# Optimization experiments

Hardware: AMD Instinct MI355X
Metric: run time of the kernel (lower is better)

The kernel has to match this reference:

```python
import jax, jax.numpy as jnp
import numpy as np

SIGMA1 = 0.1  # init kwarg s


def setup_inputs() -> dict:
    key = jax.random.key(0)
    k1, k2 = jax.random.split(key)
    N, D = 8192, 128
    fvec = jax.random.normal(k1, (N, D), dtype=jnp.float32)
    Lvec = jax.random.randint(k2, (N,), 0, 1024, dtype=jnp.int32)
    a = jnp.ones((), dtype=jnp.float32)
    return {"fvec": fvec, "Lvec": Lvec, "a": a, "IPC": 512, "bz": 8192}


def reference(fvec, Lvec, a, IPC, bz):
    # data != 'SOP' branch of HSELoss.forward (Lvec is unused on this path).
    N = fvec.shape[0]
    # F.normalize(fvec, p=2, dim=1) with eps clamp
    norm = jnp.maximum(jnp.linalg.norm(fvec, axis=1, keepdims=True), 1e-12)
    fn = fvec / norm
    # distMC: cosine-sim matmul with diagonal forced to -1
    idx = jnp.arange(N)
    Dist = (fn @ fn.T).at[idx, idx].set(-1.0)  # [N, N]

    Dd = jax.lax.stop_gradient(Dist)  # D_detach clones
    rows = idx[:, None]
    cols = idx[None, :]
    row_sel = (rows >= bz - IPC) & (rows < bz)
    # easy: mask cols [2*IPC, bz) on the last IPC rows
    easy = jnp.where(row_sel & (cols >= 2 * IPC) & (cols < bz), -1.0, Dd)
    # hard: mask cols [0, 2*IPC) and [bz-IPC, bz) on the last IPC rows
    hard_cols = (cols < 2 * IPC) | ((cols >= bz - IPC) & (cols < bz))
    hard = jnp.where(row_sel & hard_cols, -1.0, Dd)

    I_easy = jnp.argmax(easy, axis=1)  # first max index, matches torch .max(1)
    I_hard = jnp.argmax(hard, axis=1)
    VCE = Dist[idx, I_easy]
    VCH = Dist[idx, I_hard]
    T1 = jnp.stack([VCE, VCH], axis=1)[-IPC:]  # [IPC, 2]
    Prob1 = -jax.nn.log_softmax(T1 / SIGMA1, axis=1)[:, 0]
    return a * Prob1.mean()
```

## Files before the change

### kernel.cpp

```cpp
#include <hip/hip_runtime.h>
#include <hip/hip_bf16.h>
#include <math.h>

constexpr int N   = 8192;
constexpr int D   = 128;
constexpr int IPC = 512;
constexpr int BZ  = 8192;
constexpr int Q0  = BZ - IPC;
constexpr int NQ  = IPC;
constexpr int JMAX = BZ - IPC;
constexpr int JBLK = 128;
constexpr int NJB  = JMAX / JBLK;
constexpr int EASY_JB = (2 * IPC) / JBLK;
constexpr int QBLK = 64;
constexpr int NQB  = NQ / QBLK;

typedef __attribute__((ext_vector_type(8))) short short8;
typedef __attribute__((ext_vector_type(4))) float f32x4;

__global__ __launch_bounds__(256) void knorm(const float* __restrict__ f,
                                             __hip_bfloat16* __restrict__ fn) {
    int row  = (blockIdx.x * blockDim.x + threadIdx.x) >> 6;
    int lane = threadIdx.x & 63;
    const float* rp = f + (size_t)row * D;
    float2 v = *(const float2*)(rp + 2 * lane);
    float ss = v.x * v.x + v.y * v.y;
    #pragma unroll
    for (int off = 32; off > 0; off >>= 1) ss += __shfl_xor(ss, off, 64);
    float r = 1.0f / fmaxf(sqrtf(ss), 1e-12f);
    __hip_bfloat162 h;
    h.x = __float2bfloat16(v.x * r);
    h.y = __float2bfloat16(v.y * r);
    *(__hip_bfloat162*)(fn + (size_t)row * D + 2 * lane) = h;
}

__global__ __launch_bounds__(256) void kgemm(const __hip_bfloat16* __restrict__ fnorm,
                                             float* __restrict__ pm) {
    __shared__ float red[4][QBLK];

    const int tid  = threadIdx.x;
    const int lane = tid & 63;
    const int wv   = tid >> 6;
    const int jblk = blockIdx.x;
    const int qblk = blockIdx.y;
    const int row16 = lane & 15;
    const int kgrp  = lane >> 4;

    const short* fn = (const short*)fnorm;
    const short* A  = fn + (size_t)(Q0 + qblk * QBLK) * D;
    const short* B  = fn + (size_t)(jblk * JBLK + wv * 32) * D;

    f32x4 acc[4][2] = {};

    #pragma unroll
    for (int c = 0; c < 4; ++c) {
        const int ko = c * 32 + kgrp * 8;
        short8 a[4], b[2];
        #pragma unroll
        for (int g = 0; g < 4; ++g)
            a[g] = *(const short8*)(A + (g * 16 + row16) * D + ko);
        #pragma unroll
        for (int t = 0; t < 2; ++t)
            b[t] = *(const short8*)(B + (t * 16 + row16) * D + ko);
        #pragma unroll
        for (int g = 0; g < 4; ++g)
            #pragma unroll
            for (int t = 0; t < 2; ++t)
                acc[g][t] = __builtin_amdgcn_mfma_f32_16x16x32_bf16(a[g], b[t], acc[g][t], 0, 0, 0);
    }

    float vg[4][4];
    #pragma unroll
    for (int g = 0; g < 4; ++g)
        #pragma unroll
        for (int r = 0; r < 4; ++r)
            vg[g][r] = fmaxf(acc[g][0][r], acc[g][1][r]);
    #pragma unroll
    for (int off = 1; off < 16; off <<= 1)
        #pragma unroll
        for (int g = 0; g < 4; ++g)
            #pragma unroll
            for (int r = 0; r < 4; ++r)
                vg[g][r] = fmaxf(vg[g][r], __shfl_xor(vg[g][r], off, 64));

    if ((lane & 15) == 0) {
        int sub = lane >> 4;
        #pragma unroll
        for (int g = 0; g < 4; ++g)
            #pragma unroll
            for (int r = 0; r < 4; ++r)
                red[wv][g * 16 + sub * 4 + r] = vg[g][r];
    }
    __syncthreads();
    if (tid < QBLK) {
        float m = fmaxf(fmaxf(red[0][tid], red[1][tid]),
                        fmaxf(red[2][tid], red[3][tid]));
        pm[(size_t)(qblk * QBLK + tid) * NJB + jblk] = m;
    }
}

__global__ __launch_bounds__(512) void kfinal(const float* __restrict__ pm,
                                              const float* __restrict__ a_in,
                                              float* __restrict__ out) {
    __shared__ float wsum[8];
    int q = threadIdx.x;
    const float* row = pm + (size_t)q * NJB;
    float vce = -1e30f, vch = -1e30f;
    #pragma unroll
    for (int c = 0; c < EASY_JB; ++c) vce = fmaxf(vce, row[c]);
    #pragma unroll
    for (int c = EASY_JB; c < NJB; ++c) vch = fmaxf(vch, row[c]);
    float d = (vch - vce) * 10.0f;
    float p = (d > 0.0f) ? (d + log1pf(expf(-d))) : log1pf(expf(d));
    #pragma unroll
    for (int off = 32; off > 0; off >>= 1) p += __shfl_xor(p, off, 64);
    int lane = q & 63, w = q >> 6;
    if (lane == 0) wsum[w] = p;
    __syncthreads();
    if (q == 0) {
        float s = 0.0f;
        #pragma unroll
        for (int i = 0; i < 8; ++i) s += wsum[i];
        out[0] = a_in[0] * (s / (float)NQ);
    }
}

extern "C" void kernel_launch(void* const* d_in, const int* in_sizes, int n_in,
                              void* d_out, int out_size, void* d_ws, size_t ws_size,
                              hipStream_t stream) {
    const float* f = (const float*)d_in[0];
    const float* a = (const float*)d_in[2];

    __hip_bfloat16* fn = (__hip_bfloat16*)d_ws;
    float* pm = (float*)((char*)d_ws + (size_t)N * D * sizeof(__hip_bfloat16));
    float* out = (float*)d_out;

    knorm<<<N / 4, 256, 0, stream>>>(f, fn);
    dim3 g2(NJB, NQB);
    kgemm<<<g2, 256, 0, stream>>>(fn, pm);
    kfinal<<<1, 512, 0, stream>>>(pm, a, out);
}
```

Baseline: 77.18 us.

## Fuse row normalization into GEMM kernel via padded shared-memory staging

Removes the separate normalization kernel. Each GEMM block now loads its 64 query rows and 128 candidate rows as fp32, L2-normalizes them, converts to bf16, and stores them in a padded LDS tile. The MFMA operands are then read from LDS instead of global memory. This saves one launch and the bf16 workspace round-trip. In exchange, each block redundantly re-normalizes rows and reads fp32 data, which is twice the bytes of the earlier bf16 reads.

```diff
diff --git a/kernel.cpp b/kernel.cpp
--- a/kernel.cpp
+++ b/kernel.cpp
@@ -14,28 +14,14 @@
 constexpr int EASY_JB = (2 * IPC) / JBLK;
 constexpr int QBLK = 64;
 constexpr int NQB  = NQ / QBLK;
+constexpr int RSTR = 136;
 
 typedef __attribute__((ext_vector_type(8))) short short8;
 typedef __attribute__((ext_vector_type(4))) float f32x4;
 
-__global__ __launch_bounds__(256) void knorm(const float* __restrict__ f,
-                                             __hip_bfloat16* __restrict__ fn) {
-    int row  = (blockIdx.x * blockDim.x + threadIdx.x) >> 6;
-    int lane = threadIdx.x & 63;
-    const float* rp = f + (size_t)row * D;
-    float2 v = *(const float2*)(rp + 2 * lane);
-    float ss = v.x * v.x + v.y * v.y;
-    #pragma unroll
-    for (int off = 32; off > 0; off >>= 1) ss += __shfl_xor(ss, off, 64);
-    float r = 1.0f / fmaxf(sqrtf(ss), 1e-12f);
-    __hip_bfloat162 h;
-    h.x = __float2bfloat16(v.x * r);
-    h.y = __float2bfloat16(v.y * r);
-    *(__hip_bfloat162*)(fn + (size_t)row * D + 2 * lane) = h;
-}
-
-__global__ __launch_bounds__(256) void kgemm(const __hip_bfloat16* __restrict__ fnorm,
+__global__ __launch_bounds__(256) void kmain(const float* __restrict__ f,
                                              float* __restrict__ pm) {
+    __shared__ __align__(16) short S[192 * RSTR];
     __shared__ float red[4][QBLK];
 
     const int tid  = threadIdx.x;
@@ -43,25 +29,52 @@
     const int wv   = tid >> 6;
     const int jblk = blockIdx.x;
     const int qblk = blockIdx.y;
+
+    {
+        const int sub = tid & 15;
+        const int rof = tid >> 4;
+        #pragma unroll
+        for (int i = 0; i < 12; ++i) {
+            int ridx = i * 16 + rof;
+            int grow = (ridx < QBLK) ? (Q0 + qblk * QBLK + ridx)
+                                     : (jblk * JBLK + (ridx - QBLK));
+            const float* rp = f + (size_t)grow * D + sub * 8;
+            float4 v0 = *(const float4*)(rp);
+            float4 v1 = *(const float4*)(rp + 4);
+            float ss = v0.x*v0.x + v0.y*v0.y + v0.z*v0.z + v0.w*v0.w
+                     + v1.x*v1.x + v1.y*v1.y + v1.z*v1.z + v1.w*v1.w;
+            #pragma unroll
+            for (int off = 1; off < 16; off <<= 1) ss += __shfl_xor(ss, off, 64);
+            float r = 1.0f / fmaxf(sqrtf(ss), 1e-12f);
+            float sc[8] = { v0.x*r, v0.y*r, v0.z*r, v0.w*r,
+                            v1.x*r, v1.y*r, v1.z*r, v1.w*r };
+            short8 h;
+            #pragma unroll
+            for (int e = 0; e < 8; ++e) {
+                __hip_bfloat16 b = __float2bfloat16(sc[e]);
+                h[e] = *(short*)&b;
+            }
+            *(short8*)&S[ridx * RSTR + sub * 8] = h;
+        }
+    }
+    __syncthreads();
+
     const int row16 = lane & 15;
     const int kgrp  = lane >> 4;
-
-    const short* fn = (const short*)fnorm;
-    const short* A  = fn + (size_t)(Q0 + qblk * QBLK) * D;
-    const short* B  = fn + (size_t)(jblk * JBLK + wv * 32) * D;
+    const short* As = S;
+    const short* Bs = S + QBLK * RSTR + wv * 32 * RSTR;
 
     f32x4 acc[4][2] = {};
-
     #pragma unroll
     for (int c = 0; c < 4; ++c) {
         const int ko = c * 32 + kgrp * 8;
         short8 a[4], b[2];
         #pragma unroll
         for (int g = 0; g < 4; ++g)
-            a[g] = *(const short8*)(A + (g * 16 + row16) * D + ko);
+            a[g] = *(const short8*)(As + (g * 16 + row16) * RSTR + ko);
         #pragma unroll
         for (int t = 0; t < 2; ++t)
-            b[t] = *(const short8*)(B + (t * 16 + row16) * D + ko);
+            b[t] = *(const short8*)(Bs + (t * 16 + row16) * RSTR + ko);
         #pragma unroll
         for (int g = 0; g < 4; ++g)
             #pragma unroll
@@ -84,12 +97,12 @@
                 vg[g][r] = fmaxf(vg[g][r], __shfl_xor(vg[g][r], off, 64));
 
     if ((lane & 15) == 0) {
-        int sub = lane >> 4;
+        int sgrp = lane >> 4;
         #pragma unroll
         for (int g = 0; g < 4; ++g)
             #pragma unroll
             for (int r = 0; r < 4; ++r)
-                red[wv][g * 16 + sub * 4 + r] = vg[g][r];
+                red[wv][g * 16 + sgrp * 4 + r] = vg[g][r];
     }
     __syncthreads();
     if (tid < QBLK) {
@@ -131,12 +144,10 @@
     const float* f = (const float*)d_in[0];
     const float* a = (const float*)d_in[2];
 
-    __hip_bfloat16* fn = (__hip_bfloat16*)d_ws;
-    float* pm = (float*)((char*)d_ws + (size_t)N * D * sizeof(__hip_bfloat16));
+    float* pm  = (float*)d_ws;
     float* out = (float*)d_out;
 
-    knorm<<<N / 4, 256, 0, stream>>>(f, fn);
-    dim3 g2(NJB, NQB);
-    kgemm<<<g2, 256, 0, stream>>>(fn, pm);
+    dim3 g(NJB, NQB);
+    kmain<<<g, 256, 0, stream>>>(f, pm);
     kfinal<<<1, 512, 0, stream>>>(pm, a, out);
 }
```

Measured after the change: 71.72 us. -7.1%, faster.
